# Optimization experiments

Measured on AMD Instinct MI355X. Metric: run time of the kernel, lower is better.

Reference implementation:

```python
import jax, jax.numpy as jnp
import numpy as np

B, N, D = 16, 128, 128
E = N * N  # full graph: all (i,j) pairs including diagonal


def setup_inputs() -> dict:
    key = jax.random.key(0)
    k1, k2 = jax.random.split(key)
    rows = jnp.repeat(jnp.arange(N), N)
    cols = jnp.tile(jnp.arange(N), N)
    indices = jnp.broadcast_to(jnp.stack([rows, cols], -1)[None], (B, E, 2)).astype(jnp.int32)
    values = jax.random.normal(k1, (B, E, D), dtype=jnp.float32)
    mask = jnp.ones((B, E), dtype=bool)
    node_mask = jnp.ones((B, N), dtype=bool)
    # xavier_normal for [5*D, D]
    std = (2.0 / (5 * D + D)) ** 0.5
    weight = jax.random.normal(k2, (5 * D, D), dtype=jnp.float32) * std
    return {"values": values, "weight": weight, "indices": indices,
            "mask": mask, "node_mask": node_mask}


def reference(values, weight, indices, mask, node_mask):
    # _Weight._2_to_1, cfg='default', normalize=False
    b, e, d = values.shape
    n = node_mask.shape[1]
    f = values.dtype
    row = indices[..., 0]  # [B,E]
    col = indices[..., 1]  # [B,E]
    node = jnp.arange(n)

    # d(G): scatter diagonal edges (row==col) into [B,N,D]
    is_diag = (row == col) & mask
    diag_pos = jnp.where(is_diag, row, n)  # invalid -> dropped slot n
    diagonal = jnp.zeros((b, n + 1, d), f).at[jnp.arange(b)[:, None], diag_pos].add(values)[:, :n]
    V1 = diagonal  # [B,N,D]

    # masks [B,N,E]
    M_ne = node_mask[:, :, None] & mask[:, None, :]          # batch_mask
    eq_nr = node[None, :, None] == row[:, None, :]           # diag_mask(node, row)
    eq_nc = node[None, :, None] == col[:, None, :]           # diag_mask(node, col)
    M2 = (M_ne & ~eq_nc & eq_nr).astype(f)   # row-sum excluding diagonal
    M3 = (M_ne & ~eq_nr & eq_nc).astype(f)   # col-sum excluding diagonal
    M5 = (M_ne & ~eq_nr & ~eq_nc).astype(f)  # sum over edges not touching node
    V2 = jnp.einsum('bne,bed->bnd', M2, values)
    V3 = jnp.einsum('bne,bed->bnd', M3, values)
    V5 = jnp.einsum('bne,bed->bnd', M5, values)

    # V4: broadcast sum of other nodes' diagonals
    M4 = jnp.ones((n, n), f) - jnp.eye(n, dtype=f)
    V4 = jnp.einsum('ji,bid->bjd', M4, diagonal)

    V = jnp.concatenate([V1, V2, V3, V4, V5], axis=-1)  # [B,N,5D]
    return V @ weight  # [B,N,dim_out]
```

## Files before the change

### kernel.cpp

```cpp
#include <hip/hip_runtime.h>

#define Bn 16
#define Nn 128
#define Dn 128
#define En (Nn*Nn)
#define NCH 16
#define RPC 8

#define CP_SZ    ((size_t)Bn*NCH*Nn*Dn)
#define CND      ((size_t)Bn*Nn*Dn)
#define CP_OFF   ((size_t)0)
#define R_OFF    (CP_OFF + CP_SZ)
#define DG_OFF   (R_OFF + CND)

__device__ __forceinline__ void f4add(float4& a, const float4& b) {
  a.x += b.x; a.y += b.y; a.z += b.z; a.w += b.w;
}

__global__ __launch_bounds__(512) void k1(const float* __restrict__ values,
                                          float* __restrict__ ws) {
  float* Cp = ws + CP_OFF;
  float* R  = ws + R_OFF;
  float* Dg = ws + DG_OFF;
  const int chunk = blockIdx.x, b = blockIdx.y;
  const int tid  = threadIdx.x;
  const int csub = tid >> 5;
  const int d4   = tid & 31;
  const int wave = tid >> 6;
  const int lane = tid & 63;
  __shared__ float4 lred[RPC][8][32];
  float4 Cacc[8];
#pragma unroll
  for (int i = 0; i < 8; ++i) Cacc[i] = make_float4(0.f, 0.f, 0.f, 0.f);
  const float4* v4 = (const float4*)values;
  for (int rr = 0; rr < RPC; ++rr) {
    const int row = chunk * RPC + rr;
    const size_t rowbase = ((size_t)b * Nn + row) * (size_t)(Nn * (Dn / 4));
    float4 Racc = make_float4(0.f, 0.f, 0.f, 0.f);
#pragma unroll
    for (int it = 0; it < 8; ++it) {
      const int c = it * 16 + csub;
      float4 v = v4[rowbase + (size_t)c * (Dn / 4) + d4];
      f4add(Racc, v);
      f4add(Cacc[it], v);
      if (c == row)
        ((float4*)Dg)[((size_t)b * Nn + row) * (Dn / 4) + d4] = v;
    }
    float4 o;
    o.x = __shfl_xor(Racc.x, 32, 64); o.y = __shfl_xor(Racc.y, 32, 64);
    o.z = __shfl_xor(Racc.z, 32, 64); o.w = __shfl_xor(Racc.w, 32, 64);
    f4add(Racc, o);
    if (lane < 32) lred[rr][wave][lane] = Racc;
  }
  __syncthreads();
  if (tid < 256) {
    const int r = tid >> 5, dd = tid & 31;
    float4 s = lred[r][0][dd];
#pragma unroll
    for (int w = 1; w < 8; ++w) f4add(s, lred[r][w][dd]);
    ((float4*)R)[((size_t)b * Nn + (chunk * RPC + r)) * (Dn / 4) + dd] = s;
  }
#pragma unroll
  for (int it = 0; it < 8; ++it) {
    const int c = it * 16 + csub;
    ((float4*)Cp)[(((size_t)b * NCH + chunk) * Nn + c) * (Dn / 4) + d4] = Cacc[it];
  }
}

__global__ __launch_bounds__(256) void k2f(const float* __restrict__ ws,
                                           const float* __restrict__ weight,
                                           float* __restrict__ out) {
  const int tile = blockIdx.x, b = blockIdx.y;
  const int tid = threadIdx.x;
  const int n0 = tile * 8;
  const float* Cp = ws + CP_OFF;
  const float* R  = ws + R_OFF;
  const float* Dg = ws + DG_OFF;
  __shared__ float X[5][Dn][8];
  __shared__ float4 Y[8][8][32];
  __shared__ float Tp[2][128], Sp[2][128];

  const int h = tid >> 7;
  const int d = tid & 127;

  float csum[4] = {0.f, 0.f, 0.f, 0.f};
#pragma unroll
  for (int ch = 0; ch < NCH; ++ch) {
    const size_t base = (((size_t)b * NCH + ch) * Nn + n0 + h * 4) * Dn + d;
#pragma unroll
    for (int i = 0; i < 4; ++i) csum[i] += Cp[base + (size_t)i * Dn];
  }
  float t_ = 0.f, s_ = 0.f;
  const size_t bb = (size_t)b * Nn * Dn + (size_t)h * 64 * Dn + d;
#pragma unroll 16
  for (int r = 0; r < 64; ++r) {
    t_ += R [bb + (size_t)r * Dn];
    s_ += Dg[bb + (size_t)r * Dn];
  }
  Tp[h][d] = t_; Sp[h][d] = s_;
  __syncthreads();
  const float t  = Tp[0][d] + Tp[1][d];
  const float sd = Sp[0][d] + Sp[1][d];
#pragma unroll
  for (int i = 0; i < 4; ++i) {
    const int ni = h * 4 + i;
    const size_t o = ((size_t)b * Nn + (n0 + ni)) * Dn + d;
    const float dg = Dg[o], rr = R[o], cc = csum[i];
    X[0][d][ni] = dg;
    X[1][d][ni] = rr - dg;
    X[2][d][ni] = cc - dg;
    X[3][d][ni] = sd - dg;
    X[4][d][ni] = t - rr - cc + dg;
  }
  __syncthreads();

  const int d4 = tid & 31;
  const int hh = tid >> 5;
  float4 a[8];
#pragma unroll
  for (int n = 0; n < 8; ++n) a[n] = make_float4(0.f, 0.f, 0.f, 0.f);
  for (int k = 0; k < 5; ++k) {
    const float* wk = weight + (size_t)k * Dn * Dn;
#pragma unroll 4
    for (int j = 0; j < 16; ++j) {
      const int dd = hh * 16 + j;
      const float4 w = *(const float4*)&wk[(size_t)dd * Dn + d4 * 4];
      const float4 xlo = *(const float4*)&X[k][dd][0];
      const float4 xhi = *(const float4*)&X[k][dd][4];
      a[0].x += xlo.x * w.x; a[0].y += xlo.x * w.y; a[0].z += xlo.x * w.z; a[0].w += xlo.x * w.w;
      a[1].x += xlo.y * w.x; a[1].y += xlo.y * w.y; a[1].z += xlo.y * w.z; a[1].w += xlo.y * w.w;
      a[2].x += xlo.z * w.x; a[2].y += xlo.z * w.y; a[2].z += xlo.z * w.z; a[2].w += xlo.z * w.w;
      a[3].x += xlo.w * w.x; a[3].y += xlo.w * w.y; a[3].z += xlo.w * w.z; a[3].w += xlo.w * w.w;
      a[4].x += xhi.x * w.x; a[4].y += xhi.x * w.y; a[4].z += xhi.x * w.z; a[4].w += xhi.x * w.w;
      a[5].x += xhi.y * w.x; a[5].y += xhi.y * w.y; a[5].z += xhi.y * w.z; a[5].w += xhi.y * w.w;
      a[6].x += xhi.z * w.x; a[6].y += xhi.z * w.y; a[6].z += xhi.z * w.z; a[6].w += xhi.z * w.w;
      a[7].x += xhi.w * w.x; a[7].y += xhi.w * w.y; a[7].z += xhi.w * w.z; a[7].w += xhi.w * w.w;
    }
  }
#pragma unroll
  for (int n = 0; n < 8; ++n) Y[hh][n][d4] = a[n];
  __syncthreads();
  const int n = tid >> 5;
  float4 o = Y[0][n][d4];
#pragma unroll
  for (int w = 1; w < 8; ++w) f4add(o, Y[w][n][d4]);
  ((float4*)out)[((size_t)b * Nn + (n0 + n)) * (Dn / 4) + d4] = o;
}

extern "C" void kernel_launch(void* const* d_in, const int* in_sizes, int n_in,
                              void* d_out, int out_size, void* d_ws, size_t ws_size,
                              hipStream_t stream) {
  const float* values = (const float*)d_in[0];
  const float* weight = (const float*)d_in[1];
  float* ws  = (float*)d_ws;
  float* out = (float*)d_out;

  hipLaunchKernelGGL(k1,  dim3(NCH, Bn),    dim3(512), 0, stream, values, ws);
  hipLaunchKernelGGL(k2f, dim3(Nn / 8, Bn), dim3(256), 0, stream, ws, weight, out);
}
```

Baseline: 50.00 us.

## Hoist per-batch T and diagonal sums into separate kernel, halve node tile

Adds a small kernel k3 that computes, once per batch, the column sums of R and of the diagonal and stores them in workspace. Before this, every k2f block recomputed those sums itself. k2f now reads the precomputed values and handles 4 nodes per block instead of 8, which doubles the grid to 512 blocks for better occupancy on many CUs. The cost is one extra launch, and each weight element is now loaded from global memory twice as many times across blocks.

```diff
diff --git a/kernel.cpp b/kernel.cpp
--- a/kernel.cpp
+++ b/kernel.cpp
@@ -12,6 +12,8 @@
 #define CP_OFF   ((size_t)0)
 #define R_OFF    (CP_OFF + CP_SZ)
 #define DG_OFF   (R_OFF + CND)
+#define T_OFF    (DG_OFF + CND)
+#define SDG_OFF  (T_OFF + (size_t)Bn*Dn)
 
 __device__ __forceinline__ void f4add(float4& a, const float4& b) {
   a.x += b.x; a.y += b.y; a.z += b.z; a.w += b.w;
@@ -67,43 +69,46 @@
   }
 }
 
+__global__ __launch_bounds__(256) void k3(float* __restrict__ ws) {
+  const int which = blockIdx.x, b = blockIdx.y;
+  const int g = threadIdx.x >> 7, d = threadIdx.x & 127;
+  const float* src = ws + (which ? DG_OFF : R_OFF) + (size_t)b * Nn * Dn;
+  float s = 0.f;
+#pragma unroll 16
+  for (int i = 0; i < 64; ++i) s += src[(size_t)(g * 64 + i) * Dn + d];
+  __shared__ float lsum[128];
+  if (g == 1) lsum[d] = s;
+  __syncthreads();
+  if (g == 0) ws[(which ? SDG_OFF : T_OFF) + (size_t)b * Dn + d] = s + lsum[d];
+}
+
 __global__ __launch_bounds__(256) void k2f(const float* __restrict__ ws,
                                            const float* __restrict__ weight,
                                            float* __restrict__ out) {
   const int tile = blockIdx.x, b = blockIdx.y;
   const int tid = threadIdx.x;
-  const int n0 = tile * 8;
+  const int n0 = tile * 4;
   const float* Cp = ws + CP_OFF;
   const float* R  = ws + R_OFF;
   const float* Dg = ws + DG_OFF;
-  __shared__ float X[5][Dn][8];
-  __shared__ float4 Y[8][8][32];
-  __shared__ float Tp[2][128], Sp[2][128];
+  __shared__ float X[5][Dn][4];
+  __shared__ float4 Y[8][4][32];
 
   const int h = tid >> 7;
   const int d = tid & 127;
 
-  float csum[4] = {0.f, 0.f, 0.f, 0.f};
+  float csum[2] = {0.f, 0.f};
 #pragma unroll
   for (int ch = 0; ch < NCH; ++ch) {
-    const size_t base = (((size_t)b * NCH + ch) * Nn + n0 + h * 4) * Dn + d;
+    const size_t base = (((size_t)b * NCH + ch) * Nn + n0 + h * 2) * Dn + d;
+    csum[0] += Cp[base];
+    csum[1] += Cp[base + Dn];
+  }
+  const float t  = ws[T_OFF   + (size_t)b * Dn + d];
+  const float sd = ws[SDG_OFF + (size_t)b * Dn + d];
 #pragma unroll
-    for (int i = 0; i < 4; ++i) csum[i] += Cp[base + (size_t)i * Dn];
-  }
-  float t_ = 0.f, s_ = 0.f;
-  const size_t bb = (size_t)b * Nn * Dn + (size_t)h * 64 * Dn + d;
-#pragma unroll 16
-  for (int r = 0; r < 64; ++r) {
-    t_ += R [bb + (size_t)r * Dn];
-    s_ += Dg[bb + (size_t)r * Dn];
-  }
-  Tp[h][d] = t_; Sp[h][d] = s_;
-  __syncthreads();
-  const float t  = Tp[0][d] + Tp[1][d];
-  const float sd = Sp[0][d] + Sp[1][d];
-#pragma unroll
-  for (int i = 0; i < 4; ++i) {
-    const int ni = h * 4 + i;
+  for (int i = 0; i < 2; ++i) {
+    const int ni = h * 2 + i;
     const size_t o = ((size_t)b * Nn + (n0 + ni)) * Dn + d;
     const float dg = Dg[o], rr = R[o], cc = csum[i];
     X[0][d][ni] = dg;
@@ -116,35 +121,32 @@
 
   const int d4 = tid & 31;
   const int hh = tid >> 5;
-  float4 a[8];
+  float4 a[4];
 #pragma unroll
-  for (int n = 0; n < 8; ++n) a[n] = make_float4(0.f, 0.f, 0.f, 0.f);
+  for (int n = 0; n < 4; ++n) a[n] = make_float4(0.f, 0.f, 0.f, 0.f);
   for (int k = 0; k < 5; ++k) {
     const float* wk = weight + (size_t)k * Dn * Dn;
 #pragma unroll 4
     for (int j = 0; j < 16; ++j) {
       const int dd = hh * 16 + j;
       const float4 w = *(const float4*)&wk[(size_t)dd * Dn + d4 * 4];
-      const float4 xlo = *(const float4*)&X[k][dd][0];
-      const float4 xhi = *(const float4*)&X[k][dd][4];
-      a[0].x += xlo.x * w.x; a[0].y += xlo.x * w.y; a[0].z += xlo.x * w.z; a[0].w += xlo.x * w.w;
-      a[1].x += xlo.y * w.x; a[1].y += xlo.y * w.y; a[1].z += xlo.y * w.z; a[1].w += xlo.y * w.w;
-      a[2].x += xlo.z * w.x; a[2].y += xlo.z * w.y; a[2].z += xlo.z * w.z; a[2].w += xlo.z * w.w;
-      a[3].x += xlo.w * w.x; a[3].y += xlo.w * w.y; a[3].z += xlo.w * w.z; a[3].w += xlo.w * w.w;
-      a[4].x += xhi.x * w.x; a[4].y += xhi.x * w.y; a[4].z += xhi.x * w.z; a[4].w += xhi.x * w.w;
-      a[5].x += xhi.y * w.x; a[5].y += xhi.y * w.y; a[5].z += xhi.y * w.z; a[5].w += xhi.y * w.w;
-      a[6].x += xhi.z * w.x; a[6].y += xhi.z * w.y; a[6].z += xhi.z * w.z; a[6].w += xhi.z * w.w;
-      a[7].x += xhi.w * w.x; a[7].y += xhi.w * w.y; a[7].z += xhi.w * w.z; a[7].w += xhi.w * w.w;
+      const float4 x = *(const float4*)&X[k][dd][0];
+      a[0].x += x.x * w.x; a[0].y += x.x * w.y; a[0].z += x.x * w.z; a[0].w += x.x * w.w;
+      a[1].x += x.y * w.x; a[1].y += x.y * w.y; a[1].z += x.y * w.z; a[1].w += x.y * w.w;
+      a[2].x += x.z * w.x; a[2].y += x.z * w.y; a[2].z += x.z * w.z; a[2].w += x.z * w.w;
+      a[3].x += x.w * w.x; a[3].y += x.w * w.y; a[3].z += x.w * w.z; a[3].w += x.w * w.w;
     }
   }
 #pragma unroll
-  for (int n = 0; n < 8; ++n) Y[hh][n][d4] = a[n];
+  for (int n = 0; n < 4; ++n) Y[hh][n][d4] = a[n];
   __syncthreads();
-  const int n = tid >> 5;
-  float4 o = Y[0][n][d4];
+  if (tid < 128) {
+    const int n = tid >> 5;
+    float4 o = Y[0][n][d4];
 #pragma unroll
-  for (int w = 1; w < 8; ++w) f4add(o, Y[w][n][d4]);
-  ((float4*)out)[((size_t)b * Nn + (n0 + n)) * (Dn / 4) + d4] = o;
+    for (int w = 1; w < 8; ++w) f4add(o, Y[w][n][d4]);
+    ((float4*)out)[((size_t)b * Nn + (n0 + n)) * (Dn / 4) + d4] = o;
+  }
 }
 
 extern "C" void kernel_launch(void* const* d_in, const int* in_sizes, int n_in,
@@ -156,5 +158,6 @@
   float* out = (float*)d_out;
 
   hipLaunchKernelGGL(k1,  dim3(NCH, Bn),    dim3(512), 0, stream, values, ws);
-  hipLaunchKernelGGL(k2f, dim3(Nn / 8, Bn), dim3(256), 0, stream, ws, weight, out);
+  hipLaunchKernelGGL(k3,  dim3(2, Bn),      dim3(256), 0, stream, ws);
+  hipLaunchKernelGGL(k2f, dim3(Nn / 4, Bn), dim3(256), 0, stream, ws, weight, out);
 }
```

Measured after the change: 48.47 us. 3.1% less time.

## Replace per-chunk column partials with atomic reduction and precompute global sums

Applied to the files above, without the earlier changes.

The column-sum partials are no longer written as a 16-way partial buffer. Each k1 block atomically adds its column accumulators into a single zeroed [B,N,D] buffer, and a new small kernel k3 precomputes the per-batch total of row sums and diagonal sums. This cuts workspace traffic and removes the redundant per-tile reductions in k2f. The cost is a memset, an extra launch and float atomics, which make the summation order nondeterministic.

```diff
diff --git a/kernel.cpp b/kernel.cpp
--- a/kernel.cpp
+++ b/kernel.cpp
@@ -7,11 +7,12 @@
 #define NCH 16
 #define RPC 8
 
-#define CP_SZ    ((size_t)Bn*NCH*Nn*Dn)
 #define CND      ((size_t)Bn*Nn*Dn)
-#define CP_OFF   ((size_t)0)
-#define R_OFF    (CP_OFF + CP_SZ)
+#define C_OFF    ((size_t)0)
+#define R_OFF    (C_OFF + CND)
 #define DG_OFF   (R_OFF + CND)
+#define T_OFF    (DG_OFF + CND)
+#define SDG_OFF  (T_OFF + (size_t)Bn*Dn)
 
 __device__ __forceinline__ void f4add(float4& a, const float4& b) {
   a.x += b.x; a.y += b.y; a.z += b.z; a.w += b.w;
@@ -19,7 +20,7 @@
 
 __global__ __launch_bounds__(512) void k1(const float* __restrict__ values,
                                           float* __restrict__ ws) {
-  float* Cp = ws + CP_OFF;
+  float* C  = ws + C_OFF;
   float* R  = ws + R_OFF;
   float* Dg = ws + DG_OFF;
   const int chunk = blockIdx.x, b = blockIdx.y;
@@ -52,6 +53,15 @@
     f4add(Racc, o);
     if (lane < 32) lred[rr][wave][lane] = Racc;
   }
+#pragma unroll
+  for (int it = 0; it < 8; ++it) {
+    const int c = it * 16 + csub;
+    float* cp = C + ((size_t)b * Nn + c) * Dn + d4 * 4;
+    atomicAdd(cp + 0, Cacc[it].x);
+    atomicAdd(cp + 1, Cacc[it].y);
+    atomicAdd(cp + 2, Cacc[it].z);
+    atomicAdd(cp + 3, Cacc[it].w);
+  }
   __syncthreads();
   if (tid < 256) {
     const int r = tid >> 5, dd = tid & 31;
@@ -60,11 +70,19 @@
     for (int w = 1; w < 8; ++w) f4add(s, lred[r][w][dd]);
     ((float4*)R)[((size_t)b * Nn + (chunk * RPC + r)) * (Dn / 4) + dd] = s;
   }
-#pragma unroll
-  for (int it = 0; it < 8; ++it) {
-    const int c = it * 16 + csub;
-    ((float4*)Cp)[(((size_t)b * NCH + chunk) * Nn + c) * (Dn / 4) + d4] = Cacc[it];
-  }
+}
+
+__global__ __launch_bounds__(256) void k3(float* __restrict__ ws) {
+  const int which = blockIdx.x, b = blockIdx.y;
+  const int g = threadIdx.x >> 7, d = threadIdx.x & 127;
+  const float* src = ws + (which ? DG_OFF : R_OFF) + (size_t)b * Nn * Dn;
+  float s = 0.f;
+#pragma unroll 16
+  for (int i = 0; i < 64; ++i) s += src[(size_t)(g * 64 + i) * Dn + d];
+  __shared__ float lsum[128];
+  if (g == 1) lsum[d] = s;
+  __syncthreads();
+  if (g == 0) ws[(which ? SDG_OFF : T_OFF) + (size_t)b * Dn + d] = s + lsum[d];
 }
 
 __global__ __launch_bounds__(256) void k2f(const float* __restrict__ ws,
@@ -73,39 +91,21 @@
   const int tile = blockIdx.x, b = blockIdx.y;
   const int tid = threadIdx.x;
   const int n0 = tile * 8;
-  const float* Cp = ws + CP_OFF;
+  const float* C  = ws + C_OFF;
   const float* R  = ws + R_OFF;
   const float* Dg = ws + DG_OFF;
   __shared__ float X[5][Dn][8];
   __shared__ float4 Y[8][8][32];
-  __shared__ float Tp[2][128], Sp[2][128];
 
   const int h = tid >> 7;
   const int d = tid & 127;
-
-  float csum[4] = {0.f, 0.f, 0.f, 0.f};
-#pragma unroll
-  for (int ch = 0; ch < NCH; ++ch) {
-    const size_t base = (((size_t)b * NCH + ch) * Nn + n0 + h * 4) * Dn + d;
-#pragma unroll
-    for (int i = 0; i < 4; ++i) csum[i] += Cp[base + (size_t)i * Dn];
-  }
-  float t_ = 0.f, s_ = 0.f;
-  const size_t bb = (size_t)b * Nn * Dn + (size_t)h * 64 * Dn + d;
-#pragma unroll 16
-  for (int r = 0; r < 64; ++r) {
-    t_ += R [bb + (size_t)r * Dn];
-    s_ += Dg[bb + (size_t)r * Dn];
-  }
-  Tp[h][d] = t_; Sp[h][d] = s_;
-  __syncthreads();
-  const float t  = Tp[0][d] + Tp[1][d];
-  const float sd = Sp[0][d] + Sp[1][d];
+  const float t  = ws[T_OFF   + (size_t)b * Dn + d];
+  const float sd = ws[SDG_OFF + (size_t)b * Dn + d];
 #pragma unroll
   for (int i = 0; i < 4; ++i) {
     const int ni = h * 4 + i;
     const size_t o = ((size_t)b * Nn + (n0 + ni)) * Dn + d;
-    const float dg = Dg[o], rr = R[o], cc = csum[i];
+    const float dg = Dg[o], rr = R[o], cc = C[o];
     X[0][d][ni] = dg;
     X[1][d][ni] = rr - dg;
     X[2][d][ni] = cc - dg;
@@ -155,6 +155,8 @@
   float* ws  = (float*)d_ws;
   float* out = (float*)d_out;
 
+  hipMemsetAsync(ws + C_OFF, 0, CND * sizeof(float), stream);
   hipLaunchKernelGGL(k1,  dim3(NCH, Bn),    dim3(512), 0, stream, values, ws);
+  hipLaunchKernelGGL(k3,  dim3(2, Bn),      dim3(256), 0, stream, ws);
   hipLaunchKernelGGL(k2f, dim3(Nn / 8, Bn), dim3(256), 0, stream, ws, weight, out);
 }
```

Result: slower. 127.0 us (+154.1%).
